# Kernel optimization log

Measured on AMD Instinct MI355X. Metric: run time of the kernel, lower is better.

The kernel has to match this reference:

```python
import jax, jax.numpy as jnp
import numpy as np

N = 100000
E = 1600000
H = 4
NEG_SLOPE = 0.2
EPS = 1e-16


def _gat_layer(x, src, dst, edge_attr, W, We, a_src, a_dst, a_edge, b):
    # x: [N, Fin]; W: [Fin, H*C]; att vectors: [H, C]; edge_attr: [Etot, edge_dim]
    C = a_src.shape[1]
    h = (x @ W).reshape(-1, H, C)                      # [N, H, C]
    as_n = jnp.sum(h * a_src, axis=-1)                 # [N, H]
    ad_n = jnp.sum(h * a_dst, axis=-1)                 # [N, H]
    he = (edge_attr @ We).reshape(-1, H, C)            # [Etot, H, C]
    ae = jnp.sum(he * a_edge, axis=-1)                 # [Etot, H]
    alpha = as_n[src] + ad_n[dst] + ae                 # [Etot, H]
    alpha = jax.nn.leaky_relu(alpha, NEG_SLOPE)
    # softmax over incoming edges of each destination node
    amax = jax.ops.segment_max(alpha, dst, num_segments=N)
    amax = jnp.where(jnp.isfinite(amax), amax, 0.0)
    ex = jnp.exp(alpha - amax[dst])
    denom = jax.ops.segment_sum(ex, dst, num_segments=N)
    w = ex / (denom[dst] + EPS)                        # [Etot, H]
    out = jax.ops.segment_sum(w[:, :, None] * h[src], dst, num_segments=N)  # [N,H,C]
    return out.mean(axis=1) + b                        # concat=False -> head mean


def setup_inputs() -> dict:
    key = jax.random.key(0)
    ks = jax.random.split(key, 16)
    F_IN, C1, C2, ED = 64, 32, 16, 8
    s = lambda fan: 1.0 / np.sqrt(fan)
    inp = {
        "x": jax.random.normal(ks[0], (N, F_IN), jnp.float32),
        "edge_index": jax.random.randint(ks[1], (2, E), 0, N, jnp.int64),
        "edge_attr": jax.random.normal(ks[2], (E, ED), jnp.float32),
        "W1": jax.random.normal(ks[3], (F_IN, H * C1), jnp.float32) * s(F_IN),
        "We1": jax.random.normal(ks[4], (ED, H * C1), jnp.float32) * s(ED),
        "a_src1": jax.random.normal(ks[5], (H, C1), jnp.float32) * s(C1),
        "a_dst1": jax.random.normal(ks[6], (H, C1), jnp.float32) * s(C1),
        "a_edge1": jax.random.normal(ks[7], (H, C1), jnp.float32) * s(C1),
        "b1": jnp.zeros((C1,), jnp.float32),
        "W2": jax.random.normal(ks[8], (C1, H * C2), jnp.float32) * s(C1),
        "We2": jax.random.normal(ks[9], (ED, H * C2), jnp.float32) * s(ED),
        "a_src2": jax.random.normal(ks[10], (H, C2), jnp.float32) * s(C2),
        "a_dst2": jax.random.normal(ks[11], (H, C2), jnp.float32) * s(C2),
        "a_edge2": jax.random.normal(ks[12], (H, C2), jnp.float32) * s(C2),
        "b2": jnp.zeros((C2,), jnp.float32),
    }
    return inp


def reference(x, edge_index, edge_attr, W1, We1, a_src1, a_dst1, a_edge1, b1,
              W2, We2, a_src2, a_dst2, a_edge2, b2):
    # add self loops with fill_value=0 edge features (PyG fill_value=0)
    loops = jnp.arange(N, dtype=edge_index.dtype)
    src = jnp.concatenate([edge_index[0], loops])
    dst = jnp.concatenate([edge_index[1], loops])
    ea = jnp.concatenate([edge_attr, jnp.zeros((N, edge_attr.shape[1]), edge_attr.dtype)])
    h = _gat_layer(x, src, dst, ea, W1, We1, a_src1, a_dst1, a_edge1, b1)
    h = jax.nn.elu(h)
    h = _gat_layer(h, src, dst, ea, W2, We2, a_src2, a_dst2, a_edge2, b2)
    return jax.nn.elu(h)
```

## Files before the change

kernel.cpp:

```cpp
#include <hip/hip_runtime.h>
#include <hip/hip_fp16.h>
#include <math.h>

#define N_NODES 100000
#define N_EDGES 1600000
#define ETOT    (N_EDGES + N_NODES)
#define NHEAD   4
#define ED      8


__global__ void count_kernel(const int* __restrict__ ei, int* __restrict__ counts) {
    int e = blockIdx.x * 256 + threadIdx.x;
    if (e >= ETOT) return;
    int d = (e < N_EDGES) ? ei[N_EDGES + e] : (e - N_EDGES);
    atomicAdd(&counts[d], 1);
}

#define SCAN_CHUNK 1024
#define SCAN_NB    ((N_NODES + SCAN_CHUNK - 1) / SCAN_CHUNK)

__global__ void scan1_kernel(const int* __restrict__ counts, int* __restrict__ rowptr,
                             int* __restrict__ bsum) {
    __shared__ int tmp[SCAN_CHUNK];
    int t = threadIdx.x;
    int i = blockIdx.x * SCAN_CHUNK + t;
    int v = (i < N_NODES) ? counts[i] : 0;
    tmp[t] = v;
    __syncthreads();
    for (int off = 1; off < SCAN_CHUNK; off <<= 1) {
        int x = (t >= off) ? tmp[t - off] : 0;
        __syncthreads();
        tmp[t] += x;
        __syncthreads();
    }
    if (i < N_NODES) rowptr[i] = tmp[t] - v;
    if (t == SCAN_CHUNK - 1) bsum[blockIdx.x] = tmp[t];
}

__global__ void scan2_kernel(int* __restrict__ bsum) {
    if (threadIdx.x == 0 && blockIdx.x == 0) {
        int run = 0;
        for (int b = 0; b < SCAN_NB; ++b) { int t = bsum[b]; bsum[b] = run; run += t; }
    }
}

__global__ void scan3_kernel(int* __restrict__ rowptr, const int* __restrict__ bsum,
                             int* __restrict__ cursor) {
    int i = blockIdx.x * SCAN_CHUNK + threadIdx.x;
    if (i < N_NODES) {
        int v = rowptr[i] + bsum[blockIdx.x];
        rowptr[i] = v;
        cursor[i] = v;
    }
    if (i == 0) rowptr[N_NODES] = ETOT;
}

__global__ void fill_kernel(const int* __restrict__ ei, int* __restrict__ cursor,
                            int4* __restrict__ ecsr) {
    int e = blockIdx.x * 256 + threadIdx.x;
    if (e >= ETOT) return;
    int s, d;
    if (e < N_EDGES) { s = ei[e]; d = ei[N_EDGES + e]; }
    else             { s = e - N_EDGES; d = s; }
    int p = atomicAdd(&cursor[d], 1);
    ecsr[p] = make_int4(s, e, d, 0);
}


__global__ void make_M(const float* __restrict__ We, const float* __restrict__ a_edge,
                       float* __restrict__ M, int C) {
    int t = threadIdx.x;
    if (t >= ED * NHEAD) return;
    int d = t >> 2, h = t & 3;
    float s = 0.f;
    for (int c = 0; c < C; ++c) s += We[d * (NHEAD * C) + h * C + c] * a_edge[h * C + c];
    M[d * NHEAD + h] = s;
}


template <int FIN, int C, typename HT>
__global__ __launch_bounds__(256) void feat_kernel(
    const float* __restrict__ x, const float* __restrict__ W,
    const float* __restrict__ a_src, const float* __restrict__ a_dst,
    HT* __restrict__ h, float* __restrict__ as_n, float* __restrict__ ad_n) {
    constexpr int CH  = NHEAD * C;
    constexpr int TPN = CH / 4;
    constexpr int NPB = 256 / TPN;
    __shared__ float xs[NPB][FIN + 1];
    int t = threadIdx.x;
    int ln = t / TPN;
    int ct = t % TPN;
    int nbase = blockIdx.x * NPB;
    for (int i = t; i < NPB * FIN; i += 256) {
        int nn = i / FIN, dd = i % FIN;
        int gn = nbase + nn;
        xs[nn][dd] = (gn < N_NODES) ? x[(size_t)gn * FIN + dd] : 0.f;
    }
    __syncthreads();
    int n = nbase + ln;
    if (n >= N_NODES) return;
    float a0 = 0, a1 = 0, a2 = 0, a3 = 0;
    const float* wp = W + ct * 4;
#pragma unroll
    for (int dd = 0; dd < FIN; ++dd) {
        float xv = xs[ln][dd];
        float4 wv = *reinterpret_cast<const float4*>(wp + (size_t)dd * CH);
        a0 += xv * wv.x; a1 += xv * wv.y; a2 += xv * wv.z; a3 += xv * wv.w;
    }
    if constexpr (sizeof(HT) == 2) {
        __half2 p01 = __floats2half2_rn(a0, a1);
        __half2 p23 = __floats2half2_rn(a2, a3);
        __half2* hp = reinterpret_cast<__half2*>(
            reinterpret_cast<__half*>(h) + (size_t)n * CH + ct * 4);
        hp[0] = p01; hp[1] = p23;
    } else {
        *reinterpret_cast<float4*>(reinterpret_cast<float*>(h) + (size_t)n * CH + ct * 4)
            = make_float4(a0, a1, a2, a3);
    }
    int c4 = ct * 4;
    float sa = a0 * a_src[c4] + a1 * a_src[c4 + 1] + a2 * a_src[c4 + 2] + a3 * a_src[c4 + 3];
    float sd = a0 * a_dst[c4] + a1 * a_dst[c4 + 1] + a2 * a_dst[c4 + 2] + a3 * a_dst[c4 + 3];
    constexpr int GRP = C / 4;
#pragma unroll
    for (int off = GRP / 2; off > 0; off >>= 1) {
        sa += __shfl_xor(sa, off);
        sd += __shfl_xor(sd, off);
    }
    if ((ct & (GRP - 1)) == 0) {
        int head = ct / GRP;
        as_n[(size_t)n * NHEAD + head] = sa;
        ad_n[(size_t)n * NHEAD + head] = sd;
    }
}


__global__ __launch_bounds__(256) void alpha_csr(
    const int4* __restrict__ ecsr, const float* __restrict__ ea,
    const float4* __restrict__ as4, const float4* __restrict__ ad4,
    const float* __restrict__ M, float4* __restrict__ wbuf) {
    int p = blockIdx.x * 256 + threadIdx.x;
    if (p >= ETOT) return;
    int4 r = ecsr[p];
    int s = r.x, e = r.y, d = r.z;
    float4 A = as4[s];
    float4 B = ad4[d];
    float a0 = A.x + B.x, a1 = A.y + B.y, a2 = A.z + B.z, a3 = A.w + B.w;
    if (e < N_EDGES) {
        const float* er = ea + (size_t)e * ED;
        float4 E0 = *reinterpret_cast<const float4*>(er);
        float4 E1 = *reinterpret_cast<const float4*>(er + 4);
        float ev[8] = {E0.x, E0.y, E0.z, E0.w, E1.x, E1.y, E1.z, E1.w};
#pragma unroll
        for (int dd = 0; dd < 8; ++dd) {
            float xv = ev[dd];
            a0 += xv * M[dd * 4 + 0];
            a1 += xv * M[dd * 4 + 1];
            a2 += xv * M[dd * 4 + 2];
            a3 += xv * M[dd * 4 + 3];
        }
    }
    a0 = (a0 > 0.f) ? a0 : 0.2f * a0;
    a1 = (a1 > 0.f) ? a1 : 0.2f * a1;
    a2 = (a2 > 0.f) ? a2 : 0.2f * a2;
    a3 = (a3 > 0.f) ? a3 : 0.2f * a3;
    wbuf[p] = make_float4(__expf(a0), __expf(a1), __expf(a2), __expf(a3));
}


template <int C, typename HT>
__global__ __launch_bounds__(256) void gat_agg(
    const int* __restrict__ rowptr, const int4* __restrict__ ecsr,
    const float* __restrict__ wbuf, const void* __restrict__ hbuf,
    const float* __restrict__ bias, float* __restrict__ out) {
    constexpr int FPL = (NHEAD * C) / 64;
    int lane = threadIdx.x & 63;
    int n = blockIdx.x * 4 + (threadIdx.x >> 6);
    if (n >= N_NODES) return;
    int head = lane >> 4;

    const __half2* h16 = reinterpret_cast<const __half2*>(hbuf);
    const float*   h32 = reinterpret_cast<const float*>(hbuf);

    int p0 = __builtin_amdgcn_readfirstlane(rowptr[n]);
    int p1 = __builtin_amdgcn_readfirstlane(rowptr[n + 1]);

    float acc[8][FPL];
    float den[8];
#pragma unroll
    for (int j = 0; j < 8; ++j) {
        den[j] = 0.f;
#pragma unroll
        for (int k = 0; k < FPL; ++k) acc[j][k] = 0.f;
    }

    for (int p = p0; p < p1; p += 8) {
        int   sp[8];
        float w[8];
#pragma unroll
        for (int j = 0; j < 8; ++j) {
            int pp = p + j;
            bool ok = pp < p1;
            int q = ok ? pp : (p1 - 1);
            sp[j] = ecsr[q].x;
            float wv = wbuf[(size_t)q * 4 + head];
            w[j] = ok ? wv : 0.f;
        }
#pragma unroll
        for (int j = 0; j < 8; ++j) {
            float v[FPL];
            if constexpr (C == 32) {
                float2 f = __half22float2(h16[(size_t)sp[j] * 64 + lane]);
                v[0] = f.x; v[1] = f.y;
            } else {
                v[0] = h32[(size_t)sp[j] * 64 + lane];
            }
            den[j] += w[j];
#pragma unroll
            for (int k = 0; k < FPL; ++k) acc[j][k] += w[j] * v[k];
        }
    }

    float dsum = ((den[0] + den[1]) + (den[2] + den[3]))
               + ((den[4] + den[5]) + (den[6] + den[7]));
    float inv = 1.f / (dsum + 1e-16f);
    float v[FPL];
#pragma unroll
    for (int k = 0; k < FPL; ++k) {
        float a = ((acc[0][k] + acc[1][k]) + (acc[2][k] + acc[3][k]))
                + ((acc[4][k] + acc[5][k]) + (acc[6][k] + acc[7][k]));
        v[k] = a * inv;
    }
#pragma unroll
    for (int k = 0; k < FPL; ++k) {
        v[k] += __shfl_xor(v[k], 16);
        v[k] += __shfl_xor(v[k], 32);
    }
    if (lane < 16) {
#pragma unroll
        for (int k = 0; k < FPL; ++k) {
            int c = lane * FPL + k;
            float o = 0.25f * v[k] + bias[c];
            o = (o > 0.f) ? o : expm1f(o);
            out[(size_t)n * C + c] = o;
        }
    }
}


static inline size_t align_up(size_t x, size_t a) { return (x + a - 1) & ~(a - 1); }

extern "C" void kernel_launch(void* const* d_in, const int* in_sizes, int n_in,
                              void* d_out, int out_size, void* d_ws, size_t ws_size,
                              hipStream_t stream) {
    const float* x       = (const float*)d_in[0];
    const int*   ei      = (const int*)d_in[1];
    const float* ea      = (const float*)d_in[2];
    const float* W1      = (const float*)d_in[3];
    const float* We1     = (const float*)d_in[4];
    const float* a_src1  = (const float*)d_in[5];
    const float* a_dst1  = (const float*)d_in[6];
    const float* a_edge1 = (const float*)d_in[7];
    const float* b1      = (const float*)d_in[8];
    const float* W2      = (const float*)d_in[9];
    const float* We2     = (const float*)d_in[10];
    const float* a_src2  = (const float*)d_in[11];
    const float* a_dst2  = (const float*)d_in[12];
    const float* a_edge2 = (const float*)d_in[13];
    const float* b2      = (const float*)d_in[14];
    float* out = (float*)d_out;

    char* p = (char*)d_ws;
    auto take = [&](size_t bytes) { char* r = p; p += align_up(bytes, 256); return r; };
    int*    counts = (int*)take(sizeof(int) * N_NODES);
    int*    rowptr = (int*)take(sizeof(int) * (N_NODES + 1));
    int*    cursor = (int*)take(sizeof(int) * N_NODES);
    int*    bsum   = (int*)take(sizeof(int) * 128);
    int4*   ecsr   = (int4*)take(sizeof(int4) * ETOT);
    float4* wbuf   = (float4*)take(sizeof(float4) * ETOT);
    float*  as_n   = (float*)take(sizeof(float) * N_NODES * NHEAD);
    float*  ad_n   = (float*)take(sizeof(float) * N_NODES * NHEAD);
    void*   hbuf   = (void*)take((size_t)N_NODES * 128 * 2);
    float*  x2     = (float*)take(sizeof(float) * (size_t)N_NODES * 32);
    float*  M1     = (float*)take(sizeof(float) * ED * NHEAD);
    float*  M2     = (float*)take(sizeof(float) * ED * NHEAD);

    hipMemsetAsync(counts, 0, sizeof(int) * N_NODES, stream);

    int egrid = (ETOT + 255) / 256;
    count_kernel<<<egrid, 256, 0, stream>>>(ei, counts);
    scan1_kernel<<<SCAN_NB, SCAN_CHUNK, 0, stream>>>(counts, rowptr, bsum);
    scan2_kernel<<<1, 1, 0, stream>>>(bsum);
    scan3_kernel<<<SCAN_NB, SCAN_CHUNK, 0, stream>>>(rowptr, bsum, cursor);
    fill_kernel<<<egrid, 256, 0, stream>>>(ei, cursor, ecsr);

    make_M<<<1, 32, 0, stream>>>(We1, a_edge1, M1, 32);
    make_M<<<1, 32, 0, stream>>>(We2, a_edge2, M2, 16);

    int ngrid = N_NODES / 4;

    feat_kernel<64, 32, __half><<<(N_NODES + 7) / 8, 256, 0, stream>>>(
        x, W1, a_src1, a_dst1, (__half*)hbuf, as_n, ad_n);
    alpha_csr<<<egrid, 256, 0, stream>>>(ecsr, ea, (const float4*)as_n,
                                         (const float4*)ad_n, M1, wbuf);
    gat_agg<32, __half><<<ngrid, 256, 0, stream>>>(rowptr, ecsr, (const float*)wbuf,
                                                   hbuf, b1, x2);

    feat_kernel<32, 16, float><<<(N_NODES + 15) / 16, 256, 0, stream>>>(
        x2, W2, a_src2, a_dst2, (float*)hbuf, as_n, ad_n);
    alpha_csr<<<egrid, 256, 0, stream>>>(ecsr, ea, (const float4*)as_n,
                                         (const float4*)ad_n, M2, wbuf);
    gat_agg<16, float><<<ngrid, 256, 0, stream>>>(rowptr, ecsr, (const float*)wbuf,
                                                  hbuf, b2, out);
}
```

Baseline: 660.3 us.

## Fuse edge-attention terms into CSR fill and compute softmax weights inside aggregation

The CSR fill kernel now computes the edge-attribute attention terms for both layers once, packs them as fp16 next to the source index in a 32-byte record, and drops the two per-layer alpha kernels. The aggregation kernel rebuilds each edge weight on the fly from as_n[src], ad_n[dst] and the stored edge term, then applies leaky-relu and exp. This removes two edge-sized passes and the float4 weight buffer. The layer-2 features are also stored as fp16. In exchange it adds a gather of as_n per edge inside aggregation, records written with a strided partial store, and lower precision for the edge terms and layer-2 features.

```diff
diff --git a/kernel.cpp b/kernel.cpp
--- a/kernel.cpp
+++ b/kernel.cpp
@@ -55,17 +55,6 @@
     if (i == 0) rowptr[N_NODES] = ETOT;
 }
 
-__global__ void fill_kernel(const int* __restrict__ ei, int* __restrict__ cursor,
-                            int4* __restrict__ ecsr) {
-    int e = blockIdx.x * 256 + threadIdx.x;
-    if (e >= ETOT) return;
-    int s, d;
-    if (e < N_EDGES) { s = ei[e]; d = ei[N_EDGES + e]; }
-    else             { s = e - N_EDGES; d = s; }
-    int p = atomicAdd(&cursor[d], 1);
-    ecsr[p] = make_int4(s, e, d, 0);
-}
-
 
 __global__ void make_M(const float* __restrict__ We, const float* __restrict__ a_edge,
                        float* __restrict__ M, int C) {
@@ -75,6 +64,48 @@
     float s = 0.f;
     for (int c = 0; c < C; ++c) s += We[d * (NHEAD * C) + h * C + c] * a_edge[h * C + c];
     M[d * NHEAD + h] = s;
+}
+
+
+__global__ __launch_bounds__(256) void fill_kernel(
+    const int* __restrict__ ei, const float* __restrict__ ea,
+    const float* __restrict__ M1, const float* __restrict__ M2,
+    int* __restrict__ cursor, uint* __restrict__ rec) {
+    int e = blockIdx.x * 256 + threadIdx.x;
+    if (e >= ETOT) return;
+    int s, d;
+    float a10 = 0, a11 = 0, a12 = 0, a13 = 0;
+    float a20 = 0, a21 = 0, a22 = 0, a23 = 0;
+    if (e < N_EDGES) {
+        s = ei[e]; d = ei[N_EDGES + e];
+        const float* er = ea + (size_t)e * ED;
+        float4 E0 = *reinterpret_cast<const float4*>(er);
+        float4 E1 = *reinterpret_cast<const float4*>(er + 4);
+        float ev[8] = {E0.x, E0.y, E0.z, E0.w, E1.x, E1.y, E1.z, E1.w};
+#pragma unroll
+        for (int dd = 0; dd < 8; ++dd) {
+            float xv = ev[dd];
+            a10 += xv * M1[dd * 4 + 0]; a11 += xv * M1[dd * 4 + 1];
+            a12 += xv * M1[dd * 4 + 2]; a13 += xv * M1[dd * 4 + 3];
+            a20 += xv * M2[dd * 4 + 0]; a21 += xv * M2[dd * 4 + 1];
+            a22 += xv * M2[dd * 4 + 2]; a23 += xv * M2[dd * 4 + 3];
+        }
+    } else {
+        s = e - N_EDGES; d = s;
+    }
+    int p = atomicAdd(&cursor[d], 1);
+    __half2 h10 = __floats2half2_rn(a10, a11);
+    __half2 h11 = __floats2half2_rn(a12, a13);
+    __half2 h20 = __floats2half2_rn(a20, a21);
+    __half2 h21 = __floats2half2_rn(a22, a23);
+    uint4 lo;
+    lo.x = (uint)s;
+    lo.y = *reinterpret_cast<uint*>(&h10);
+    lo.z = *reinterpret_cast<uint*>(&h11);
+    lo.w = *reinterpret_cast<uint*>(&h20);
+    uint* rp = rec + (size_t)p * 8;
+    *reinterpret_cast<uint4*>(rp) = lo;
+    rp[4] = *reinterpret_cast<uint*>(&h21);
 }
 
 
@@ -134,52 +165,20 @@
 }
 
 
-__global__ __launch_bounds__(256) void alpha_csr(
-    const int4* __restrict__ ecsr, const float* __restrict__ ea,
-    const float4* __restrict__ as4, const float4* __restrict__ ad4,
-    const float* __restrict__ M, float4* __restrict__ wbuf) {
-    int p = blockIdx.x * 256 + threadIdx.x;
-    if (p >= ETOT) return;
-    int4 r = ecsr[p];
-    int s = r.x, e = r.y, d = r.z;
-    float4 A = as4[s];
-    float4 B = ad4[d];
-    float a0 = A.x + B.x, a1 = A.y + B.y, a2 = A.z + B.z, a3 = A.w + B.w;
-    if (e < N_EDGES) {
-        const float* er = ea + (size_t)e * ED;
-        float4 E0 = *reinterpret_cast<const float4*>(er);
-        float4 E1 = *reinterpret_cast<const float4*>(er + 4);
-        float ev[8] = {E0.x, E0.y, E0.z, E0.w, E1.x, E1.y, E1.z, E1.w};
-#pragma unroll
-        for (int dd = 0; dd < 8; ++dd) {
-            float xv = ev[dd];
-            a0 += xv * M[dd * 4 + 0];
-            a1 += xv * M[dd * 4 + 1];
-            a2 += xv * M[dd * 4 + 2];
-            a3 += xv * M[dd * 4 + 3];
-        }
-    }
-    a0 = (a0 > 0.f) ? a0 : 0.2f * a0;
-    a1 = (a1 > 0.f) ? a1 : 0.2f * a1;
-    a2 = (a2 > 0.f) ? a2 : 0.2f * a2;
-    a3 = (a3 > 0.f) ? a3 : 0.2f * a3;
-    wbuf[p] = make_float4(__expf(a0), __expf(a1), __expf(a2), __expf(a3));
-}
-
-
-template <int C, typename HT>
+template <int C, int AEOFF>
 __global__ __launch_bounds__(256) void gat_agg(
-    const int* __restrict__ rowptr, const int4* __restrict__ ecsr,
-    const float* __restrict__ wbuf, const void* __restrict__ hbuf,
-    const float* __restrict__ bias, float* __restrict__ out) {
+    const int* __restrict__ rowptr, const char* __restrict__ rec,
+    const __half* __restrict__ hbuf, const float* __restrict__ as_n,
+    const float* __restrict__ ad_n, const float* __restrict__ bias,
+    float* __restrict__ out) {
     constexpr int FPL = (NHEAD * C) / 64;
     int lane = threadIdx.x & 63;
     int n = blockIdx.x * 4 + (threadIdx.x >> 6);
     if (n >= N_NODES) return;
     int head = lane >> 4;
 
-    const __half2* h16 = reinterpret_cast<const __half2*>(hbuf);
-    const float*   h32 = reinterpret_cast<const float*>(hbuf);
+    float ad = ad_n[(size_t)n * NHEAD + head];
+    const __half2* h2p = reinterpret_cast<const __half2*>(hbuf);
 
     int p0 = __builtin_amdgcn_readfirstlane(rowptr[n]);
     int p1 = __builtin_amdgcn_readfirstlane(rowptr[n + 1]);
@@ -201,18 +200,22 @@
             int pp = p + j;
             bool ok = pp < p1;
             int q = ok ? pp : (p1 - 1);
-            sp[j] = ecsr[q].x;
-            float wv = wbuf[(size_t)q * 4 + head];
+            const char* rp = rec + (size_t)q * 32;
+            sp[j] = *reinterpret_cast<const int*>(rp);
+            __half aeh = *reinterpret_cast<const __half*>(rp + AEOFF + 2 * head);
+            float a = as_n[(size_t)sp[j] * NHEAD + head] + ad + __half2float(aeh);
+            a = (a > 0.f) ? a : 0.2f * a;
+            float wv = __expf(a);
             w[j] = ok ? wv : 0.f;
         }
 #pragma unroll
         for (int j = 0; j < 8; ++j) {
             float v[FPL];
             if constexpr (C == 32) {
-                float2 f = __half22float2(h16[(size_t)sp[j] * 64 + lane]);
+                float2 f = __half22float2(h2p[(size_t)sp[j] * 64 + lane]);
                 v[0] = f.x; v[1] = f.y;
             } else {
-                v[0] = h32[(size_t)sp[j] * 64 + lane];
+                v[0] = __half2float(hbuf[(size_t)sp[j] * 64 + lane]);
             }
             den[j] += w[j];
 #pragma unroll
@@ -271,18 +274,17 @@
 
     char* p = (char*)d_ws;
     auto take = [&](size_t bytes) { char* r = p; p += align_up(bytes, 256); return r; };
-    int*    counts = (int*)take(sizeof(int) * N_NODES);
-    int*    rowptr = (int*)take(sizeof(int) * (N_NODES + 1));
-    int*    cursor = (int*)take(sizeof(int) * N_NODES);
-    int*    bsum   = (int*)take(sizeof(int) * 128);
-    int4*   ecsr   = (int4*)take(sizeof(int4) * ETOT);
-    float4* wbuf   = (float4*)take(sizeof(float4) * ETOT);
-    float*  as_n   = (float*)take(sizeof(float) * N_NODES * NHEAD);
-    float*  ad_n   = (float*)take(sizeof(float) * N_NODES * NHEAD);
-    void*   hbuf   = (void*)take((size_t)N_NODES * 128 * 2);
-    float*  x2     = (float*)take(sizeof(float) * (size_t)N_NODES * 32);
-    float*  M1     = (float*)take(sizeof(float) * ED * NHEAD);
-    float*  M2     = (float*)take(sizeof(float) * ED * NHEAD);
+    int*   counts = (int*)take(sizeof(int) * N_NODES);
+    int*   rowptr = (int*)take(sizeof(int) * (N_NODES + 1));
+    int*   cursor = (int*)take(sizeof(int) * N_NODES);
+    int*   bsum   = (int*)take(sizeof(int) * 128);
+    char*  rec    = (char*)take((size_t)ETOT * 32);
+    float* as_n   = (float*)take(sizeof(float) * N_NODES * NHEAD);
+    float* ad_n   = (float*)take(sizeof(float) * N_NODES * NHEAD);
+    __half* hbuf  = (__half*)take((size_t)N_NODES * 128 * 2);
+    float* x2     = (float*)take(sizeof(float) * (size_t)N_NODES * 32);
+    float* M1     = (float*)take(sizeof(float) * ED * NHEAD);
+    float* M2     = (float*)take(sizeof(float) * ED * NHEAD);
 
     hipMemsetAsync(counts, 0, sizeof(int) * N_NODES, stream);
 
@@ -291,24 +293,19 @@
     scan1_kernel<<<SCAN_NB, SCAN_CHUNK, 0, stream>>>(counts, rowptr, bsum);
     scan2_kernel<<<1, 1, 0, stream>>>(bsum);
     scan3_kernel<<<SCAN_NB, SCAN_CHUNK, 0, stream>>>(rowptr, bsum, cursor);
-    fill_kernel<<<egrid, 256, 0, stream>>>(ei, cursor, ecsr);
 
     make_M<<<1, 32, 0, stream>>>(We1, a_edge1, M1, 32);
     make_M<<<1, 32, 0, stream>>>(We2, a_edge2, M2, 16);
 
+    fill_kernel<<<egrid, 256, 0, stream>>>(ei, ea, M1, M2, cursor, (uint*)rec);
+
     int ngrid = N_NODES / 4;
 
     feat_kernel<64, 32, __half><<<(N_NODES + 7) / 8, 256, 0, stream>>>(
-        x, W1, a_src1, a_dst1, (__half*)hbuf, as_n, ad_n);
-    alpha_csr<<<egrid, 256, 0, stream>>>(ecsr, ea, (const float4*)as_n,
-                                         (const float4*)ad_n, M1, wbuf);
-    gat_agg<32, __half><<<ngrid, 256, 0, stream>>>(rowptr, ecsr, (const float*)wbuf,
-                                                   hbuf, b1, x2);
-
-    feat_kernel<32, 16, float><<<(N_NODES + 15) / 16, 256, 0, stream>>>(
-        x2, W2, a_src2, a_dst2, (float*)hbuf, as_n, ad_n);
-    alpha_csr<<<egrid, 256, 0, stream>>>(ecsr, ea, (const float4*)as_n,
-                                         (const float4*)ad_n, M2, wbuf);
-    gat_agg<16, float><<<ngrid, 256, 0, stream>>>(rowptr, ecsr, (const float*)wbuf,
-                                                  hbuf, b2, out);
-}
+        x, W1, a_src1, a_dst1, hbuf, as_n, ad_n);
+    gat_agg<32, 4><<<ngrid, 256, 0, stream>>>(rowptr, rec, hbuf, as_n, ad_n, b1, x2);
+
+    feat_kernel<32, 16, __half><<<(N_NODES + 15) / 16, 256, 0, stream>>>(
+        x2, W2, a_src2, a_dst2, hbuf, as_n, ad_n);
+    gat_agg<16, 12><<<ngrid, 256, 0, stream>>>(rowptr, rec, hbuf, as_n, ad_n, b2, out);
+}
```

Result: faster. 597.8 us (-9.5%).
